# Optimization experiments

Measured on AMD Instinct MI355X. Metric: run time of the kernel, lower is better.

## Reference

```python
import jax, jax.numpy as jnp
import numpy as np

B, H, K, D = 4096, 3, 32768, 128


def setup_inputs() -> dict:
    key = jax.random.key(0)
    k_in, k_emb = jax.random.split(key)
    inputs = jax.random.normal(k_in, (B, 1, D), dtype=jnp.float32)
    # xavier-uniform-ish init with per-head decay 0.5**h (gain 6.0), as in the module
    ks = jax.random.split(k_emb, H)
    tables = []
    for h in range(H):
        gain = 6.0 * (0.5 ** h)
        bound = gain * np.sqrt(6.0 / (K + D))
        tables.append(jax.random.uniform(ks[h], (K, D), jnp.float32, -bound, bound))
    emb = jnp.stack(tables, axis=0)  # [H, K, D]
    return {"inputs": inputs, "emb": emb}


def reference(inputs, emb):
    # Eval-mode HRQ forward: per-head negative squared-L2 distances to the
    # codebook on the running residual, hard argmax assignment, summed codes.
    x = inputs[:, 0, :]                      # [B, D]
    n_heads = emb.shape[0]
    resid = x
    quantized = jnp.zeros_like(x)
    codes = []
    for h in range(n_heads):
        W = emb[h]                            # [K, D]
        # -(||r||^2 + ||w||^2 - 2 r.w)  -> argmax == nearest code
        dists = -(jnp.sum(resid * resid, axis=1, keepdims=True)
                  + jnp.sum(W * W, axis=1)
                  - 2.0 * resid @ W.T)        # [B, K]
        c = jnp.argmax(dists, axis=-1)        # [B]
        q = jnp.take(W, c, axis=0)            # onehot(c) @ W == gather
        resid = resid - q
        quantized = quantized + q
        codes.append(c)
    loss = jnp.zeros(x.shape[0], dtype=inputs.dtype)
    return loss, quantized.reshape(inputs.shape), jnp.stack(codes, axis=1)
```

## Files before the change

kernel.cpp:

```cpp
#include <hip/hip_runtime.h>
#include <math.h>

#define NB 4096
#define NH 3
#define NK 32768
#define ND 128
#define KA 256
#define KB 256
#define RB 128
#define CS 16
#define CPB (NK / CS)
#define CI 128
#define NCI (CPB / CI)

typedef _Float16 half8_t __attribute__((ext_vector_type(8)));
typedef _Float16 half2_t __attribute__((ext_vector_type(2)));
typedef float f32x4 __attribute__((ext_vector_type(4)));
typedef __attribute__((address_space(1))) const unsigned int gu32_t;
typedef __attribute__((address_space(3))) unsigned int lu32_t;

__global__ __launch_bounds__(64) void init_kernel(const float* __restrict__ inp,
                                                  float* __restrict__ resid,
                                                  float* __restrict__ rr,
                                                  float* __restrict__ out,
                                                  _Float16* __restrict__ Aext) {
  int row = blockIdx.x;
  int lane = threadIdx.x;
  const float2* ip = (const float2*)(inp + row * ND);
  float2 v = ip[lane];
  ((float2*)(resid + row * ND))[lane] = v;
  ((float2*)(out + NB + row * ND))[lane] = make_float2(0.f, 0.f);
  if (lane == 0) out[row] = 0.f;
  _Float16 h0 = (_Float16)v.x, h1 = (_Float16)v.y;
  _Float16 l0 = (_Float16)(v.x - (float)h0), l1 = (_Float16)(v.y - (float)h1);
  half2_t h = {h0, h1}, l = {l0, l1};
  _Float16* base = Aext + (size_t)row * KA;
  *(half2_t*)(base + 2 * lane) = h;
  *(half2_t*)(base + 128 + 2 * lane) = l;
  float s = v.x * v.x + v.y * v.y;
  #pragma unroll
  for (int m = 32; m; m >>= 1) s += __shfl_xor(s, m, 64);
  if (lane == 0) rr[row] = s;
}

__global__ __launch_bounds__(256) void norms_kernel(const float* __restrict__ emb,
                                                    float* __restrict__ norms) {
  int row = blockIdx.x * 4 + (threadIdx.x >> 6);
  int lane = threadIdx.x & 63;
  const float2* wp = (const float2*)(emb + (size_t)row * ND);
  float2 v = wp[lane];
  float s = v.x * v.x + v.y * v.y;
  #pragma unroll
  for (int m = 32; m; m >>= 1) s += __shfl_xor(s, m, 64);
  if (lane == 0) norms[row] = s;
}

__global__ __launch_bounds__(256) void split_w_all_kernel(const float* __restrict__ emb,
                                                          _Float16* __restrict__ Bext) {
  const int head = blockIdx.x >> 11;
  const int cg = blockIdx.x & 2047;
  const int n_lo = threadIdx.x & 15;
  const int c = threadIdx.x >> 4;
  const int n = cg * 16 + n_lo;

  const float4* wp = (const float4*)(emb + (size_t)head * NK * ND + (size_t)n * ND + c * 8);
  float4 v0 = wp[0], v1 = wp[1];
  float xv[8] = {v0.x, v0.y, v0.z, v0.w, v1.x, v1.y, v1.z, v1.w};
  half8_t h, l;
  #pragma unroll
  for (int j = 0; j < 8; ++j) {
    _Float16 hh = (_Float16)xv[j];
    h[j] = hh;
    l[j] = (_Float16)(xv[j] - (float)hh);
  }
  const int ks0 = c >> 2;
  const int klo = c & 3;
  _Float16* base = Bext + (size_t)head * NK * KB + (size_t)(cg >> 2) * 16384 +
                   (cg & 3) * 512 + klo * 128 + n_lo * 8;
  *(half8_t*)(base + ks0 * 2048) = h;
  *(half8_t*)(base + (4 + ks0) * 2048) = l;
}

__global__ __launch_bounds__(512, 4) void score_mfma_kernel(
    const _Float16* __restrict__ Aext, const _Float16* __restrict__ Bext,
    const float* __restrict__ rr, const float* __restrict__ normh,
    float* __restrict__ partial_s, int* __restrict__ partial_i) {
  __shared__ __align__(16) _Float16 Ash[RB * KA];
  __shared__ __align__(16) float rrsh[RB];

  const int bid = blockIdx.x;
  const int cs = bid & (CS - 1);
  const int rowb = bid >> 4;
  const int rowBase = rowb * RB;
  const int colBase0 = cs * CPB;

  const int tid = threadIdx.x;
  const int lane = tid & 63;
  const int wn = tid >> 6;
  const int wc = wn & 3;
  const int wr = wn >> 2;
  const int l15 = lane & 15;
  const int q = lane >> 4;

  {
    const int p = wn >> 1;
    const int mh = (wn & 1) * 64;
    const int mrow = lane >> 3;
    const int cg = (lane & 7) ^ (mrow & 7);
    #pragma unroll
    for (int i = 0; i < 8; ++i) {
      const int m0 = mh + i * 8;
      const _Float16* gA = Aext + (size_t)(rowBase + m0 + mrow) * KA + p * 64 + cg * 8;
      __builtin_amdgcn_global_load_lds((gu32_t*)gA, (lu32_t*)&Ash[(p * 128 + m0) * 64], 16, 0, 0);
    }
  }
  if (tid < RB) rrsh[tid] = rr[rowBase + tid];

  int aaddr0[4];
  #pragma unroll
  for (int mt = 0; mt < 4; ++mt) {
    const int m = wr * 64 + mt * 16 + l15;
    const int slot = q ^ (m & 7);
    aaddr0[mt] = (m * 8 + slot) * 16;
  }

  float bs[16];
  int bi[16];
  #pragma unroll
  for (int t = 0; t < 16; ++t) { bs[t] = -INFINITY; bi[t] = 0x7fffffff; }

  __syncthreads();

  #pragma unroll 1
  for (int ci = NCI - 1; ci >= 0; --ci) {
    const int ncol = colBase0 + ci * CI + wc * 32;
    const unsigned int boff = (unsigned int)(ncol >> 6) * 16384u +
                              ((unsigned int)(ncol >> 4) & 3u) * 512u +
                              (unsigned int)lane * 8u;

    float nw[2];
    #pragma unroll
    for (int tn = 0; tn < 2; ++tn) nw[tn] = normh[ncol + tn * 16 + l15];

    f32x4 acc[4][2];
    #pragma unroll
    for (int i = 0; i < 4; ++i) {
      acc[i][0] = (f32x4){0.f, 0.f, 0.f, 0.f};
      acc[i][1] = (f32x4){0.f, 0.f, 0.f, 0.f};
    }

    #pragma unroll 2
    for (int kc = 0; kc < 4; ++kc) {
      half8_t bh[2], bl[2];
      #pragma unroll
      for (int tn = 0; tn < 2; ++tn) {
        bh[tn] = *(const half8_t*)(Bext + boff + (unsigned int)(kc * 2048 + tn * 512));
        bl[tn] = *(const half8_t*)(Bext + boff + (unsigned int)((4 + kc) * 2048 + tn * 512));
      }
      const int axor = (kc & 1) << 6;
      const int abase = (kc >> 1) * 16384;
      __builtin_amdgcn_s_setprio(1);
      #pragma unroll
      for (int mt = 0; mt < 4; ++mt) {
        const char* ap = (const char*)Ash + ((aaddr0[mt] ^ axor) + abase);
        half8_t ah = *(const half8_t*)ap;
        half8_t al = *(const half8_t*)(ap + 32768);
        acc[mt][0] = __builtin_amdgcn_mfma_f32_16x16x32_f16(ah, bh[0], acc[mt][0], 0, 0, 0);
        acc[mt][1] = __builtin_amdgcn_mfma_f32_16x16x32_f16(ah, bh[1], acc[mt][1], 0, 0, 0);
        acc[mt][0] = __builtin_amdgcn_mfma_f32_16x16x32_f16(al, bh[0], acc[mt][0], 0, 0, 0);
        acc[mt][1] = __builtin_amdgcn_mfma_f32_16x16x32_f16(al, bh[1], acc[mt][1], 0, 0, 0);
        acc[mt][0] = __builtin_amdgcn_mfma_f32_16x16x32_f16(ah, bl[0], acc[mt][0], 0, 0, 0);
        acc[mt][1] = __builtin_amdgcn_mfma_f32_16x16x32_f16(ah, bl[1], acc[mt][1], 0, 0, 0);
      }
      __builtin_amdgcn_s_setprio(0);
    }

    #pragma unroll
    for (int tn = 1; tn >= 0; --tn) {
      const float nwv = nw[tn];
      const int cidx = ncol + tn * 16 + l15;
      #pragma unroll
      for (int mt = 0; mt < 4; ++mt) {
        const f32x4 rvv = *(const f32x4*)&rrsh[wr * 64 + mt * 16 + q * 4];
        #pragma unroll
        for (int reg = 0; reg < 4; ++reg) {
          const int s = mt * 4 + reg;
          float t1 = rvv[reg] + nwv;
          float v = fmaf(2.0f, acc[mt][tn][reg], -t1);
          if (v >= bs[s]) { bs[s] = v; bi[s] = cidx; }
        }
      }
    }
  }

  __syncthreads();
  float* red_s = (float*)Ash;
  int* red_i = (int*)Ash + RB * 4;
  #pragma unroll
  for (int t = 0; t < 16; ++t) {
    float s = bs[t];
    int ii = bi[t];
    #pragma unroll
    for (int mask = 1; mask <= 8; mask <<= 1) {
      float os = __shfl_xor(s, mask, 64);
      int oi = __shfl_xor(ii, mask, 64);
      if (os > s || (os == s && oi < ii)) { s = os; ii = oi; }
    }
    if (l15 == 0) {
      const int rloc = wr * 64 + (t >> 2) * 16 + q * 4 + (t & 3);
      red_s[rloc * 4 + wc] = s;
      red_i[rloc * 4 + wc] = ii;
    }
  }
  __syncthreads();
  if (tid < RB) {
    float s0 = red_s[tid * 4];
    int i0 = red_i[tid * 4];
    #pragma unroll
    for (int x = 1; x < 4; ++x) {
      float sx = red_s[tid * 4 + x];
      int ix = red_i[tid * 4 + x];
      if (sx > s0 || (sx == s0 && ix < i0)) { s0 = sx; i0 = ix; }
    }
    partial_s[(size_t)(rowBase + tid) * CS + cs] = s0;
    partial_i[(size_t)(rowBase + tid) * CS + cs] = i0;
  }
}

__global__ __launch_bounds__(64) void reduce_update_kernel(const float* __restrict__ embh,
                                                           float* __restrict__ resid,
                                                           float* __restrict__ rr,
                                                           const float* __restrict__ ps,
                                                           const int* __restrict__ pi,
                                                           float* __restrict__ out,
                                                           _Float16* __restrict__ Aext, int h) {
  int row = blockIdx.x;
  int lane = threadIdx.x;
  float bs = -INFINITY;
  int bi = 0x7fffffff;
  if (lane < CS) {
    bs = ps[(size_t)row * CS + lane];
    bi = pi[(size_t)row * CS + lane];
  }
  #pragma unroll
  for (int m = 8; m; m >>= 1) {
    float os = __shfl_xor(bs, m, 64);
    int oi = __shfl_xor(bi, m, 64);
    if (os > bs || (os == bs && oi < bi)) { bs = os; bi = oi; }
  }
  int c = __shfl(bi, 0, 64);
  if (lane == 0) out[NB + NB * ND + row * NH + h] = (float)c;

  const float* wv = embh + (size_t)c * ND;
  float q0 = wv[lane], q1 = wv[lane + 64];
  float r0 = resid[row * ND + lane] - q0;
  float r1 = resid[row * ND + lane + 64] - q1;
  resid[row * ND + lane] = r0;
  resid[row * ND + lane + 64] = r1;
  out[NB + row * ND + lane] += q0;
  out[NB + row * ND + lane + 64] += q1;

  _Float16 h0 = (_Float16)r0, l0 = (_Float16)(r0 - (float)h0);
  _Float16 h1 = (_Float16)r1, l1 = (_Float16)(r1 - (float)h1);
  _Float16* ab = Aext + (size_t)row * KA;
  ab[lane] = h0;       ab[lane + 64] = h1;
  ab[128 + lane] = l0; ab[128 + lane + 64] = l1;

  float s = r0 * r0 + r1 * r1;
  #pragma unroll
  for (int m = 32; m; m >>= 1) s += __shfl_xor(s, m, 64);
  if (lane == 0) rr[row] = s;
}

extern "C" void kernel_launch(void* const* d_in, const int* in_sizes, int n_in,
                              void* d_out, int out_size, void* d_ws, size_t ws_size,
                              hipStream_t stream) {
  const float* inp = (const float*)d_in[0];
  const float* emb = (const float*)d_in[1];
  float* out = (float*)d_out;

  float* resid = (float*)d_ws;
  float* rr = resid + NB * ND;
  float* norms = rr + NB;
  float* ps = norms + NH * NK;
  int* pi = (int*)(ps + (size_t)NB * CS);
  _Float16* Aext = (_Float16*)(pi + (size_t)NB * CS);
  _Float16* Bext = Aext + (size_t)NB * KA;

  hipLaunchKernelGGL(init_kernel, dim3(NB), dim3(64), 0, stream, inp, resid, rr, out, Aext);
  hipLaunchKernelGGL(norms_kernel, dim3(NH * NK / 4), dim3(256), 0, stream, emb, norms);
  hipLaunchKernelGGL(split_w_all_kernel, dim3(NH * NK / 16), dim3(256), 0, stream, emb, Bext);
  for (int h = 0; h < NH; ++h) {
    hipLaunchKernelGGL(score_mfma_kernel, dim3((NB / RB) * CS), dim3(512), 0, stream,
                       Aext, Bext + (size_t)h * NK * KB, rr, norms + (size_t)h * NK, ps, pi);
    hipLaunchKernelGGL(reduce_update_kernel, dim3(NB), dim3(64), 0, stream,
                       emb + (size_t)h * NK * ND, resid, rr, ps, pi, out, Aext, h);
  }
}
```

Before: 402.4 us.

## Switch score GEMM to 32x32x16 MFMA with repacked B and packed argmax indices

Moves the split-fp16 score GEMM from 16x16x32 to 32x32x16 MFMA tiles. The B codebook layout and the A shared-memory swizzle are rewritten to match the new operand fragments. The running argmax now keeps 4-bit chunk indices packed into integers instead of full column indices, which cuts register use for the larger accumulators. The goal is fewer MFMA and LDS instructions per output and lower register pressure; in exchange the data layout and index reconstruction become more complex.

```diff
diff --git a/kernel.cpp b/kernel.cpp
--- a/kernel.cpp
+++ b/kernel.cpp
@@ -16,8 +16,11 @@
 typedef _Float16 half8_t __attribute__((ext_vector_type(8)));
 typedef _Float16 half2_t __attribute__((ext_vector_type(2)));
 typedef float f32x4 __attribute__((ext_vector_type(4)));
+typedef float f32x16 __attribute__((ext_vector_type(16)));
 typedef __attribute__((address_space(1))) const unsigned int gu32_t;
 typedef __attribute__((address_space(3))) unsigned int lu32_t;
+
+#define MFMA32(A_, B_, C_) __builtin_amdgcn_mfma_f32_32x32x16_f16((A_), (B_), (C_), 0, 0, 0)
 
 __global__ __launch_bounds__(64) void init_kernel(const float* __restrict__ inp,
                                                   float* __restrict__ resid,
@@ -57,28 +60,34 @@
 
 __global__ __launch_bounds__(256) void split_w_all_kernel(const float* __restrict__ emb,
                                                           _Float16* __restrict__ Bext) {
-  const int head = blockIdx.x >> 11;
-  const int cg = blockIdx.x & 2047;
-  const int n_lo = threadIdx.x & 15;
-  const int c = threadIdx.x >> 4;
-  const int n = cg * 16 + n_lo;
-
-  const float4* wp = (const float4*)(emb + (size_t)head * NK * ND + (size_t)n * ND + c * 8);
-  float4 v0 = wp[0], v1 = wp[1];
-  float xv[8] = {v0.x, v0.y, v0.z, v0.w, v1.x, v1.y, v1.z, v1.w};
-  half8_t h, l;
-  #pragma unroll
-  for (int j = 0; j < 8; ++j) {
-    _Float16 hh = (_Float16)xv[j];
-    h[j] = hh;
-    l[j] = (_Float16)(xv[j] - (float)hh);
-  }
-  const int ks0 = c >> 2;
-  const int klo = c & 3;
-  _Float16* base = Bext + (size_t)head * NK * KB + (size_t)(cg >> 2) * 16384 +
-                   (cg & 3) * 512 + klo * 128 + n_lo * 8;
-  *(half8_t*)(base + ks0 * 2048) = h;
-  *(half8_t*)(base + (4 + ks0) * 2048) = l;
+  const int head = blockIdx.x >> 10;
+  const int g = blockIdx.x & 1023;
+  const int coll = threadIdx.x & 31;
+  const int idx = threadIdx.x >> 5;
+  const int n = g * 32 + coll;
+
+  _Float16* gb = Bext + (size_t)head * NK * KB + (size_t)g * 8192;
+  const float* src = emb + (size_t)head * NK * ND + (size_t)n * ND;
+
+  #pragma unroll
+  for (int iter = 0; iter < 2; ++iter) {
+    const int kh = idx + iter * 8;
+    const int ks = kh >> 1, hi = kh & 1;
+    const int k = ks * 16 + hi * 8;
+    const float4* wp = (const float4*)(src + k);
+    float4 v0 = wp[0], v1 = wp[1];
+    float xv[8] = {v0.x, v0.y, v0.z, v0.w, v1.x, v1.y, v1.z, v1.w};
+    half8_t h, l;
+    #pragma unroll
+    for (int j = 0; j < 8; ++j) {
+      _Float16 hh = (_Float16)xv[j];
+      h[j] = hh;
+      l[j] = (_Float16)(xv[j] - (float)hh);
+    }
+    const int lanef = hi * 32 + coll;
+    *(half8_t*)(gb + ks * 512 + lanef * 8) = h;
+    *(half8_t*)(gb + (8 + ks) * 512 + lanef * 8) = l;
+  }
 }
 
 __global__ __launch_bounds__(512, 4) void score_mfma_kernel(
@@ -99,117 +108,127 @@
   const int wn = tid >> 6;
   const int wc = wn & 3;
   const int wr = wn >> 2;
-  const int l15 = lane & 15;
-  const int q = lane >> 4;
+  const int cl = lane & 31;
+  const int hi = lane >> 5;
 
   {
-    const int p = wn >> 1;
-    const int mh = (wn & 1) * 64;
-    const int mrow = lane >> 3;
-    const int cg = (lane & 7) ^ (mrow & 7);
     #pragma unroll
     for (int i = 0; i < 8; ++i) {
-      const int m0 = mh + i * 8;
-      const _Float16* gA = Aext + (size_t)(rowBase + m0 + mrow) * KA + p * 64 + cg * 8;
-      __builtin_amdgcn_global_load_lds((gu32_t*)gA, (lu32_t*)&Ash[(p * 128 + m0) * 64], 16, 0, 0);
+      const int m0 = wn * 16 + i * 2;
+      const int ml = m0 + hi;
+      const int c = cl ^ (ml & 31);
+      const _Float16* gA = Aext + (size_t)(rowBase + ml) * KA + c * 8;
+      __builtin_amdgcn_global_load_lds((gu32_t*)gA, (lu32_t*)&Ash[m0 * 256], 16, 0, 0);
     }
   }
   if (tid < RB) rrsh[tid] = rr[rowBase + tid];
 
-  int aaddr0[4];
-  #pragma unroll
-  for (int mt = 0; mt < 4; ++mt) {
-    const int m = wr * 64 + mt * 16 + l15;
-    const int slot = q ^ (m & 7);
-    aaddr0[mt] = (m * 8 + slot) * 16;
-  }
-
-  float bs[16];
-  int bi[16];
-  #pragma unroll
-  for (int t = 0; t < 16; ++t) { bs[t] = -INFINITY; bi[t] = 0x7fffffff; }
+  int Q[2];
+  #pragma unroll
+  for (int t = 0; t < 2; ++t) {
+    const int ml = wr * 64 + t * 32 + cl;
+    Q[t] = (ml * 512 + (ml & 31) * 16) ^ (hi * 16);
+  }
+
+  float bs[32];
+  int pk[4];
+  #pragma unroll
+  for (int t = 0; t < 32; ++t) bs[t] = -INFINITY;
+  #pragma unroll
+  for (int t = 0; t < 4; ++t) pk[t] = 0;
 
   __syncthreads();
+
+  const f32x16 Z = {0.f, 0.f, 0.f, 0.f, 0.f, 0.f, 0.f, 0.f,
+                    0.f, 0.f, 0.f, 0.f, 0.f, 0.f, 0.f, 0.f};
+  const char* AshB = (const char*)Ash;
 
   #pragma unroll 1
   for (int ci = NCI - 1; ci >= 0; --ci) {
     const int ncol = colBase0 + ci * CI + wc * 32;
-    const unsigned int boff = (unsigned int)(ncol >> 6) * 16384u +
-                              ((unsigned int)(ncol >> 4) & 3u) * 512u +
-                              (unsigned int)lane * 8u;
-
-    float nw[2];
-    #pragma unroll
-    for (int tn = 0; tn < 2; ++tn) nw[tn] = normh[ncol + tn * 16 + l15];
-
-    f32x4 acc[4][2];
-    #pragma unroll
-    for (int i = 0; i < 4; ++i) {
-      acc[i][0] = (f32x4){0.f, 0.f, 0.f, 0.f};
-      acc[i][1] = (f32x4){0.f, 0.f, 0.f, 0.f};
-    }
-
+    const char* bp = (const char*)Bext +
+                     ((unsigned)(ncol >> 5) * 16384u + (unsigned)lane * 16u);
+    const float nw = normh[ncol + cl];
+
+    f32x16 acc0, acc1;
+    {
+      half8_t bh = *(const half8_t*)(bp);
+      half8_t bl = *(const half8_t*)(bp + 8 * 1024);
+      half8_t a0h = *(const half8_t*)(AshB + Q[0]);
+      half8_t a1h = *(const half8_t*)(AshB + Q[1]);
+      half8_t a0l = *(const half8_t*)(AshB + (Q[0] ^ 256));
+      half8_t a1l = *(const half8_t*)(AshB + (Q[1] ^ 256));
+      __builtin_amdgcn_s_setprio(1);
+      acc0 = MFMA32(a0h, bh, Z);
+      acc1 = MFMA32(a1h, bh, Z);
+      acc0 = MFMA32(a0l, bh, acc0);
+      acc1 = MFMA32(a1l, bh, acc1);
+      acc0 = MFMA32(a0h, bl, acc0);
+      acc1 = MFMA32(a1h, bl, acc1);
+      __builtin_amdgcn_s_setprio(0);
+    }
     #pragma unroll 2
-    for (int kc = 0; kc < 4; ++kc) {
-      half8_t bh[2], bl[2];
-      #pragma unroll
-      for (int tn = 0; tn < 2; ++tn) {
-        bh[tn] = *(const half8_t*)(Bext + boff + (unsigned int)(kc * 2048 + tn * 512));
-        bl[tn] = *(const half8_t*)(Bext + boff + (unsigned int)((4 + kc) * 2048 + tn * 512));
-      }
-      const int axor = (kc & 1) << 6;
-      const int abase = (kc >> 1) * 16384;
+    for (int ks = 1; ks < 8; ++ks) {
+      half8_t bh = *(const half8_t*)(bp + ks * 1024);
+      half8_t bl = *(const half8_t*)(bp + (8 + ks) * 1024);
+      half8_t a0h = *(const half8_t*)(AshB + (Q[0] ^ (ks * 32)));
+      half8_t a1h = *(const half8_t*)(AshB + (Q[1] ^ (ks * 32)));
+      half8_t a0l = *(const half8_t*)(AshB + (Q[0] ^ (ks * 32) ^ 256));
+      half8_t a1l = *(const half8_t*)(AshB + (Q[1] ^ (ks * 32) ^ 256));
       __builtin_amdgcn_s_setprio(1);
-      #pragma unroll
-      for (int mt = 0; mt < 4; ++mt) {
-        const char* ap = (const char*)Ash + ((aaddr0[mt] ^ axor) + abase);
-        half8_t ah = *(const half8_t*)ap;
-        half8_t al = *(const half8_t*)(ap + 32768);
-        acc[mt][0] = __builtin_amdgcn_mfma_f32_16x16x32_f16(ah, bh[0], acc[mt][0], 0, 0, 0);
-        acc[mt][1] = __builtin_amdgcn_mfma_f32_16x16x32_f16(ah, bh[1], acc[mt][1], 0, 0, 0);
-        acc[mt][0] = __builtin_amdgcn_mfma_f32_16x16x32_f16(al, bh[0], acc[mt][0], 0, 0, 0);
-        acc[mt][1] = __builtin_amdgcn_mfma_f32_16x16x32_f16(al, bh[1], acc[mt][1], 0, 0, 0);
-        acc[mt][0] = __builtin_amdgcn_mfma_f32_16x16x32_f16(ah, bl[0], acc[mt][0], 0, 0, 0);
-        acc[mt][1] = __builtin_amdgcn_mfma_f32_16x16x32_f16(ah, bl[1], acc[mt][1], 0, 0, 0);
-      }
+      acc0 = MFMA32(a0h, bh, acc0);
+      acc1 = MFMA32(a1h, bh, acc1);
+      acc0 = MFMA32(a0l, bh, acc0);
+      acc1 = MFMA32(a1l, bh, acc1);
+      acc0 = MFMA32(a0h, bl, acc0);
+      acc1 = MFMA32(a1h, bl, acc1);
       __builtin_amdgcn_s_setprio(0);
     }
 
-    #pragma unroll
-    for (int tn = 1; tn >= 0; --tn) {
-      const float nwv = nw[tn];
-      const int cidx = ncol + tn * 16 + l15;
-      #pragma unroll
-      for (int mt = 0; mt < 4; ++mt) {
-        const f32x4 rvv = *(const f32x4*)&rrsh[wr * 64 + mt * 16 + q * 4];
-        #pragma unroll
-        for (int reg = 0; reg < 4; ++reg) {
-          const int s = mt * 4 + reg;
-          float t1 = rvv[reg] + nwv;
-          float v = fmaf(2.0f, acc[mt][tn][reg], -t1);
-          if (v >= bs[s]) { bs[s] = v; bi[s] = cidx; }
-        }
-      }
-    }
+    int vci[8];
+    #pragma unroll
+    for (int j = 0; j < 8; ++j) vci[j] = ci << (4 * j);
+#define FOLD_TILE(T_, ACC_)                                                    \
+    _Pragma("unroll")                                                          \
+    for (int g = 0; g < 4; ++g) {                                              \
+      const f32x4 r4 = *(const f32x4*)&rrsh[wr * 64 + (T_)*32 + hi * 4 + g * 8]; \
+      _Pragma("unroll")                                                        \
+      for (int j = 0; j < 4; ++j) {                                            \
+        const int r = g * 4 + j;                                               \
+        const int s = (T_)*16 + r;                                             \
+        float t1 = r4[j] + nw;                     \
+        float v = fmaf(2.0f, (ACC_)[r], -t1);       \
+        bool u = (v >= bs[s]);                                                 \
+        bs[s] = u ? v : bs[s];                                                 \
+        int upd = (pk[s >> 3] & ~(0xF << ((s & 7) * 4))) | vci[s & 7];         \
+        pk[s >> 3] = u ? upd : pk[s >> 3];                                     \
+      }                                                                        \
+    }
+    FOLD_TILE(0, acc0)
+    FOLD_TILE(1, acc1)
+#undef FOLD_TILE
   }
 
   __syncthreads();
   float* red_s = (float*)Ash;
   int* red_i = (int*)Ash + RB * 4;
-  #pragma unroll
-  for (int t = 0; t < 16; ++t) {
-    float s = bs[t];
-    int ii = bi[t];
-    #pragma unroll
-    for (int mask = 1; mask <= 8; mask <<= 1) {
-      float os = __shfl_xor(s, mask, 64);
+  const int cbase = colBase0 + wc * 32 + cl;
+  #pragma unroll
+  for (int s = 0; s < 32; ++s) {
+    float v = bs[s];
+    int ciS = (pk[s >> 3] >> ((s & 7) * 4)) & 15;
+    int ii = cbase + ciS * CI;
+    #pragma unroll
+    for (int mask = 1; mask <= 16; mask <<= 1) {
+      float os = __shfl_xor(v, mask, 64);
       int oi = __shfl_xor(ii, mask, 64);
-      if (os > s || (os == s && oi < ii)) { s = os; ii = oi; }
-    }
-    if (l15 == 0) {
-      const int rloc = wr * 64 + (t >> 2) * 16 + q * 4 + (t & 3);
-      red_s[rloc * 4 + wc] = s;
-      red_i[rloc * 4 + wc] = ii;
+      if (os > v || (os == v && oi < ii)) { v = os; ii = oi; }
+    }
+    if (cl == 0) {
+      const int t = s >> 4, r = s & 15;
+      const int row = wr * 64 + t * 32 + (r & 3) + 8 * (r >> 2) + 4 * hi;
+      red_s[row * 4 + wc] = v;
+      red_i[row * 4 + wc] = ii;
     }
   }
   __syncthreads();
@@ -289,7 +308,7 @@
 
   hipLaunchKernelGGL(init_kernel, dim3(NB), dim3(64), 0, stream, inp, resid, rr, out, Aext);
   hipLaunchKernelGGL(norms_kernel, dim3(NH * NK / 4), dim3(256), 0, stream, emb, norms);
-  hipLaunchKernelGGL(split_w_all_kernel, dim3(NH * NK / 16), dim3(256), 0, stream, emb, Bext);
+  hipLaunchKernelGGL(split_w_all_kernel, dim3(NH * NK / 32), dim3(256), 0, stream, emb, Bext);
   for (int h = 0; h < NH; ++h) {
     hipLaunchKernelGGL(score_mfma_kernel, dim3((NB / RB) * CS), dim3(512), 0, stream,
                        Aext, Bext + (size_t)h * NK * KB, rr, norms + (size_t)h * NK, ps, pi);
```

Result: slower. 1.521 ms (+277.9%).

## Halve score row tile to 64 and software-pipeline B fragment loads

Applied to the files above, without the earlier changes.

Shrinks the score kernel's row block from 128 to 64 rows, with 4 waves of 256 threads each owning a 32-column slice, and launches twice as many blocks. It also adds register double-buffering of the B (codebook) fragments, prefetching the next k-chunk and the next column chunk while MFMAs run on the current one, and seeds the accumulator directly from zero. This is meant to hide global-load latency of B and raise occupancy via smaller LDS use per block. In exchange, each B fragment is reused across half as many rows, doubling codebook traffic from L2/HBM, and the prefetch buffers add register pressure.

```diff
diff --git a/kernel.cpp b/kernel.cpp
--- a/kernel.cpp
+++ b/kernel.cpp
@@ -7,7 +7,7 @@
 #define ND 128
 #define KA 256
 #define KB 256
-#define RB 128
+#define RB 64
 #define CS 16
 #define CPB (NK / CS)
 #define CI 128
@@ -81,7 +81,7 @@
   *(half8_t*)(base + (4 + ks0) * 2048) = l;
 }
 
-__global__ __launch_bounds__(512, 4) void score_mfma_kernel(
+__global__ __launch_bounds__(256, 2) void score_mfma_kernel(
     const _Float16* __restrict__ Aext, const _Float16* __restrict__ Bext,
     const float* __restrict__ rr, const float* __restrict__ normh,
     float* __restrict__ partial_s, int* __restrict__ partial_i) {
@@ -97,21 +97,19 @@
   const int tid = threadIdx.x;
   const int lane = tid & 63;
   const int wn = tid >> 6;
-  const int wc = wn & 3;
-  const int wr = wn >> 2;
   const int l15 = lane & 15;
   const int q = lane >> 4;
 
   {
-    const int p = wn >> 1;
-    const int mh = (wn & 1) * 64;
     const int mrow = lane >> 3;
     const int cg = (lane & 7) ^ (mrow & 7);
     #pragma unroll
     for (int i = 0; i < 8; ++i) {
-      const int m0 = mh + i * 8;
+      int wc = wn * 8 + i;
+      int p = wc >> 3;
+      int m0 = (wc & 7) * 8;
       const _Float16* gA = Aext + (size_t)(rowBase + m0 + mrow) * KA + p * 64 + cg * 8;
-      __builtin_amdgcn_global_load_lds((gu32_t*)gA, (lu32_t*)&Ash[(p * 128 + m0) * 64], 16, 0, 0);
+      __builtin_amdgcn_global_load_lds((gu32_t*)gA, (lu32_t*)&Ash[(p * 64 + m0) * 64], 16, 0, 0);
     }
   }
   if (tid < RB) rrsh[tid] = rr[rowBase + tid];
@@ -119,8 +117,8 @@
   int aaddr0[4];
   #pragma unroll
   for (int mt = 0; mt < 4; ++mt) {
-    const int m = wr * 64 + mt * 16 + l15;
-    const int slot = q ^ (m & 7);
+    int m = mt * 16 + l15;
+    int slot = q ^ (m & 7);
     aaddr0[mt] = (m * 8 + slot) * 16;
   }
 
@@ -129,42 +127,73 @@
   #pragma unroll
   for (int t = 0; t < 16; ++t) { bs[t] = -INFINITY; bi[t] = 0x7fffffff; }
 
+  unsigned bo = (unsigned)((colBase0 + (NCI - 1) * CI + wn * 32) >> 6) * 16384u +
+                (((unsigned)(colBase0 + (NCI - 1) * CI + wn * 32) >> 4) & 3u) * 512u +
+                (unsigned)lane * 8u;
+  half8_t bh[2], bl[2];
+  #pragma unroll
+  for (int tn = 0; tn < 2; ++tn) {
+    bh[tn] = *(const half8_t*)(Bext + bo + (unsigned)(tn * 512));
+    bl[tn] = *(const half8_t*)(Bext + bo + (unsigned)(8192 + tn * 512));
+  }
+
   __syncthreads();
+
+  const f32x4 Z = {0.f, 0.f, 0.f, 0.f};
 
   #pragma unroll 1
   for (int ci = NCI - 1; ci >= 0; --ci) {
-    const int ncol = colBase0 + ci * CI + wc * 32;
-    const unsigned int boff = (unsigned int)(ncol >> 6) * 16384u +
-                              ((unsigned int)(ncol >> 4) & 3u) * 512u +
-                              (unsigned int)lane * 8u;
+    const int ncol = colBase0 + ci * CI + wn * 32;
+    const int ci_n = (ci > 0) ? ci - 1 : 0;
+    const int ncol_n = colBase0 + ci_n * CI + wn * 32;
+    const unsigned bon = (unsigned)(ncol_n >> 6) * 16384u +
+                         (((unsigned)ncol_n >> 4) & 3u) * 512u + (unsigned)lane * 8u;
 
     float nw[2];
     #pragma unroll
     for (int tn = 0; tn < 2; ++tn) nw[tn] = normh[ncol + tn * 16 + l15];
 
     f32x4 acc[4][2];
-    #pragma unroll
-    for (int i = 0; i < 4; ++i) {
-      acc[i][0] = (f32x4){0.f, 0.f, 0.f, 0.f};
-      acc[i][1] = (f32x4){0.f, 0.f, 0.f, 0.f};
-    }
-
-    #pragma unroll 2
-    for (int kc = 0; kc < 4; ++kc) {
-      half8_t bh[2], bl[2];
+    half8_t nh[2], nl[2];
+
+    {
       #pragma unroll
       for (int tn = 0; tn < 2; ++tn) {
-        bh[tn] = *(const half8_t*)(Bext + boff + (unsigned int)(kc * 2048 + tn * 512));
-        bl[tn] = *(const half8_t*)(Bext + boff + (unsigned int)((4 + kc) * 2048 + tn * 512));
+        nh[tn] = *(const half8_t*)(Bext + bo + (unsigned)(2048 + tn * 512));
+        nl[tn] = *(const half8_t*)(Bext + bo + (unsigned)(2048 + 8192 + tn * 512));
+      }
+      __builtin_amdgcn_s_setprio(1);
+      #pragma unroll
+      for (int mt = 0; mt < 4; ++mt) {
+        half8_t ah = *(const half8_t*)((const char*)Ash + aaddr0[mt]);
+        half8_t al = *(const half8_t*)((const char*)Ash + aaddr0[mt] + 16384);
+        acc[mt][0] = __builtin_amdgcn_mfma_f32_16x16x32_f16(ah, bh[0], Z, 0, 0, 0);
+        acc[mt][1] = __builtin_amdgcn_mfma_f32_16x16x32_f16(ah, bh[1], Z, 0, 0, 0);
+        acc[mt][0] = __builtin_amdgcn_mfma_f32_16x16x32_f16(al, bh[0], acc[mt][0], 0, 0, 0);
+        acc[mt][1] = __builtin_amdgcn_mfma_f32_16x16x32_f16(al, bh[1], acc[mt][1], 0, 0, 0);
+        acc[mt][0] = __builtin_amdgcn_mfma_f32_16x16x32_f16(ah, bl[0], acc[mt][0], 0, 0, 0);
+        acc[mt][1] = __builtin_amdgcn_mfma_f32_16x16x32_f16(ah, bl[1], acc[mt][1], 0, 0, 0);
+      }
+      __builtin_amdgcn_s_setprio(0);
+      bh[0] = nh[0]; bh[1] = nh[1];
+      bl[0] = nl[0]; bl[1] = nl[1];
+    }
+
+    #pragma unroll
+    for (int kc = 1; kc < 4; ++kc) {
+      const unsigned po = (kc < 3) ? bo + (unsigned)((kc + 1) * 2048) : bon;
+      #pragma unroll
+      for (int tn = 0; tn < 2; ++tn) {
+        nh[tn] = *(const half8_t*)(Bext + po + (unsigned)(tn * 512));
+        nl[tn] = *(const half8_t*)(Bext + po + (unsigned)(8192 + tn * 512));
       }
       const int axor = (kc & 1) << 6;
-      const int abase = (kc >> 1) * 16384;
+      const int abase = (kc >> 1) * 8192;
       __builtin_amdgcn_s_setprio(1);
       #pragma unroll
       for (int mt = 0; mt < 4; ++mt) {
-        const char* ap = (const char*)Ash + ((aaddr0[mt] ^ axor) + abase);
-        half8_t ah = *(const half8_t*)ap;
-        half8_t al = *(const half8_t*)(ap + 32768);
+        half8_t ah = *(const half8_t*)((const char*)Ash + ((aaddr0[mt] ^ axor) + abase));
+        half8_t al = *(const half8_t*)((const char*)Ash + ((aaddr0[mt] ^ axor) + abase + 16384));
         acc[mt][0] = __builtin_amdgcn_mfma_f32_16x16x32_f16(ah, bh[0], acc[mt][0], 0, 0, 0);
         acc[mt][1] = __builtin_amdgcn_mfma_f32_16x16x32_f16(ah, bh[1], acc[mt][1], 0, 0, 0);
         acc[mt][0] = __builtin_amdgcn_mfma_f32_16x16x32_f16(al, bh[0], acc[mt][0], 0, 0, 0);
@@ -173,6 +202,8 @@
         acc[mt][1] = __builtin_amdgcn_mfma_f32_16x16x32_f16(ah, bl[1], acc[mt][1], 0, 0, 0);
       }
       __builtin_amdgcn_s_setprio(0);
+      bh[0] = nh[0]; bh[1] = nh[1];
+      bl[0] = nl[0]; bl[1] = nl[1];
     }
 
     #pragma unroll
@@ -181,7 +212,7 @@
       const int cidx = ncol + tn * 16 + l15;
       #pragma unroll
       for (int mt = 0; mt < 4; ++mt) {
-        const f32x4 rvv = *(const f32x4*)&rrsh[wr * 64 + mt * 16 + q * 4];
+        const f32x4 rvv = *(const f32x4*)&rrsh[mt * 16 + q * 4];
         #pragma unroll
         for (int reg = 0; reg < 4; ++reg) {
           const int s = mt * 4 + reg;
@@ -191,6 +222,7 @@
         }
       }
     }
+    bo = bon;
   }
 
   __syncthreads();
@@ -207,9 +239,9 @@
       if (os > s || (os == s && oi < ii)) { s = os; ii = oi; }
     }
     if (l15 == 0) {
-      const int rloc = wr * 64 + (t >> 2) * 16 + q * 4 + (t & 3);
-      red_s[rloc * 4 + wc] = s;
-      red_i[rloc * 4 + wc] = ii;
+      int rloc = (t >> 2) * 16 + q * 4 + (t & 3);
+      red_s[rloc * 4 + wn] = s;
+      red_i[rloc * 4 + wn] = ii;
     }
   }
   __syncthreads();
@@ -291,7 +323,7 @@
   hipLaunchKernelGGL(norms_kernel, dim3(NH * NK / 4), dim3(256), 0, stream, emb, norms);
   hipLaunchKernelGGL(split_w_all_kernel, dim3(NH * NK / 16), dim3(256), 0, stream, emb, Bext);
   for (int h = 0; h < NH; ++h) {
-    hipLaunchKernelGGL(score_mfma_kernel, dim3((NB / RB) * CS), dim3(512), 0, stream,
+    hipLaunchKernelGGL(score_mfma_kernel, dim3((NB / RB) * CS), dim3(256), 0, stream,
                        Aext, Bext + (size_t)h * NK * KB, rr, norms + (size_t)h * NK, ps, pi);
     hipLaunchKernelGGL(reduce_update_kernel, dim3(NB), dim3(64), 0, stream,
                        emb + (size_t)h * NK * ND, resid, rr, ps, pi, out, Aext, h);
```

Measured after the change: 423.2 us. 5.2% more time.
